# Optimization experiments

Measured on AMD Instinct MI355X. Metric: run time of the kernel, lower is better.

## Reference

```python
import jax, jax.numpy as jnp
import numpy as np

B, S, D, H = 2, 2048, 1024, 16
HD = D // H  # head_dim = 64
ROPE_BASE = 10000.0


def apply_rope(x, positions):
    # x: [B, S, H, HD], positions: [B, S] int. Rotate-half RoPE.
    d = x.shape[-1]
    inv_freq = 1.0 / (ROPE_BASE ** (jnp.arange(0, d, 2, dtype=jnp.float32) / d))  # [d/2]
    ang = positions[..., None].astype(jnp.float32) * inv_freq  # [B, S, d/2]
    cos = jnp.cos(ang)[:, :, None, :]
    sin = jnp.sin(ang)[:, :, None, :]
    x1, x2 = jnp.split(x, 2, axis=-1)
    return jnp.concatenate([x1 * cos - x2 * sin, x2 * cos + x1 * sin], axis=-1).astype(x.dtype)


def setup_inputs() -> dict:
    key = jax.random.key(0)
    k1, k2, k3 = jax.random.split(key, 3)
    inputs = jax.random.normal(k1, (B, S, D), dtype=jnp.float32)
    # nn.Linear weights [out_features, in_features]
    W_in = jax.random.normal(k2, (3 * D, D), dtype=jnp.float32) * (1.0 / np.sqrt(D))
    W_out = jax.random.normal(k3, (D, D), dtype=jnp.float32) * (1.0 / np.sqrt(D))
    positions = jnp.tile(jnp.arange(S, dtype=jnp.int32)[None, :], (B, 1))  # [B, S]
    return {"inputs": inputs, "positions": positions, "W_in": W_in, "W_out": W_out}


def reference(inputs, positions, W_in, W_out):
    # fused QKV projection: [B, S, 3D], head-major layout per rearrange '(heads qkv)'
    qkv = jnp.einsum('bsd,ed->bse', inputs, W_in)
    qkv = qkv.reshape(B, S, H, 3 * HD)
    q, k, v = jnp.split(qkv, 3, axis=-1)  # each [B, S, H, HD]
    q = apply_rope(q, positions)
    k = apply_rope(k, positions)
    # einsum_attention (inference path): scale query, full masked softmax
    q = q / jnp.sqrt(jnp.asarray(HD, dtype=q.dtype))
    scores = jnp.einsum('bqhd,bkhd->bhqk', q, k)  # [B, H, S, S]
    mask = (jnp.arange(S)[None, None, :] <= positions[:, :, None])[:, None, :, :]  # [B,1,S,S]
    big_neg = jnp.finfo(scores.dtype).min
    scores = jnp.where(mask, scores, big_neg)
    attn = jax.nn.softmax(scores, axis=-1)
    x = jnp.einsum('bhqk,bkhd->bqhd', attn, v).reshape(B, S, D)
    return jnp.einsum('bsd,ed->bse', x, W_out)
```

## Files before the change

kernel.cpp:

```cpp
#include <hip/hip_runtime.h>
#include <stdint.h>
#include <math.h>

#define B_ 2
#define S_ 2048
#define D_ 1024
#define H_ 16
#define HD_ 64
#define KVBLK 64

typedef __bf16 bf16_t;
typedef __bf16 bf16x4 __attribute__((ext_vector_type(4)));
typedef __bf16 bf16x8 __attribute__((ext_vector_type(8)));
typedef float f32x4 __attribute__((ext_vector_type(4)));
typedef float f32x16 __attribute__((ext_vector_type(16)));
typedef float float4v __attribute__((ext_vector_type(4)));

#define L2E 1.4426950408889634f
#define NINF (-__builtin_inff())

__device__ __forceinline__ void gload_lds16(const bf16_t* g, bf16_t* l) {
  __builtin_amdgcn_global_load_lds((const __attribute__((address_space(1))) void*)g,
                                   (__attribute__((address_space(3))) void*)l, 16, 0, 0);
}

__device__ __forceinline__ uint32_t packbf(float a, float b) {
  union { __bf16 h[2]; uint32_t u; } cvt;
  cvt.h[0] = (__bf16)a; cvt.h[1] = (__bf16)b;
  return cvt.u;
}

__global__ void cast_bf16_kernel(const float* __restrict__ src, bf16_t* __restrict__ dst, int n4) {
  int i = blockIdx.x * blockDim.x + threadIdx.x;
  int stride = gridDim.x * blockDim.x;
  for (; i < n4; i += stride) {
    float4v f = *(const float4v*)(src + (size_t)i * 4);
    bf16x4 o;
    o[0] = (__bf16)f[0]; o[1] = (__bf16)f[1]; o[2] = (__bf16)f[2]; o[3] = (__bf16)f[3];
    *(bf16x4*)(dst + (size_t)i * 4) = o;
  }
}

template <typename OutT>
__global__ __launch_bounds__(256) void gemm_bt(const bf16_t* __restrict__ A,
                                               const bf16_t* __restrict__ Bm,
                                               OutT* __restrict__ C,
                                               int M, int N, int K) {
  __shared__ bf16_t As[128 * 32];
  __shared__ bf16_t Bs[128 * 32];
  const int t = threadIdx.x;
  const int lane = t & 63, wave = t >> 6;
  const int wr = wave >> 1, wc = wave & 1;
  const int qr = lane & 15, g = lane >> 4;
  const int bm = blockIdx.x, bn = blockIdx.y;

  f32x4 acc[4][4];
#pragma unroll
  for (int m = 0; m < 4; m++)
#pragma unroll
    for (int n = 0; n < 4; n++) acc[m][n] = (f32x4){0.f, 0.f, 0.f, 0.f};

  const bf16_t* Abase = A + (size_t)(bm * 128) * K;
  const bf16_t* Bbase = Bm + (size_t)(bn * 128) * K;
  const int srow = t >> 2;
  const int scol = (t & 3) * 8;

  for (int kk = 0; kk < K; kk += 32) {
    gload_lds16(Abase + (size_t)srow * K + kk + scol,        As + t * 8);
    gload_lds16(Abase + (size_t)(srow + 64) * K + kk + scol, As + 2048 + t * 8);
    gload_lds16(Bbase + (size_t)srow * K + kk + scol,        Bs + t * 8);
    gload_lds16(Bbase + (size_t)(srow + 64) * K + kk + scol, Bs + 2048 + t * 8);
    __syncthreads();
    bf16x8 a[4], b[4];
#pragma unroll
    for (int m = 0; m < 4; m++)
      a[m] = *(const bf16x8*)(As + (wr * 64 + m * 16 + qr) * 32 + g * 8);
#pragma unroll
    for (int n = 0; n < 4; n++)
      b[n] = *(const bf16x8*)(Bs + (wc * 64 + n * 16 + qr) * 32 + g * 8);
#pragma unroll
    for (int m = 0; m < 4; m++)
#pragma unroll
      for (int n = 0; n < 4; n++)
        acc[m][n] = __builtin_amdgcn_mfma_f32_16x16x32_bf16(a[m], b[n], acc[m][n], 0, 0, 0);
    __syncthreads();
  }

#pragma unroll
  for (int m = 0; m < 4; m++) {
    int row0 = bm * 128 + wr * 64 + m * 16 + g * 4;
#pragma unroll
    for (int n = 0; n < 4; n++) {
      int col = bn * 128 + wc * 64 + n * 16 + qr;
#pragma unroll
      for (int r = 0; r < 4; r++)
        C[(size_t)(row0 + r) * N + col] = (OutT)acc[m][n][r];
    }
  }
}

template <typename OutT>
__global__ __launch_bounds__(512, 2) void gemm256(const bf16_t* __restrict__ A,
                                                  const bf16_t* __restrict__ Bm,
                                                  OutT* __restrict__ C,
                                                  int M, int N, int K) {
  __shared__ bf16_t As[2][256 * 64];
  __shared__ bf16_t Bs[2][256 * 64];
  const int t = threadIdx.x;
  const int lane = t & 63, wid = t >> 6;
  const int qr = lane & 15, g = lane >> 4;
  const int wm = wid >> 2, wn = wid & 3;
  const int bm = blockIdx.x, bn = blockIdx.y;
  const int NT = K >> 6;

  const bf16_t* Ab = A + (size_t)(bm * 256) * K;
  const bf16_t* Bb = Bm + (size_t)(bn * 256) * K;

  const bf16_t* srcA[4];
  const bf16_t* srcB[4];
  int ldsOff[4];
#pragma unroll
  for (int i = 0; i < 4; i++) {
    int e = t + 512 * i;
    int row = e >> 3, cs = e & 7;
    int gcol = (cs ^ (row & 7)) * 8;
    srcA[i] = Ab + (size_t)row * K + gcol;
    srcB[i] = Bb + (size_t)row * K + gcol;
    ldsOff[i] = e * 8;
  }

  f32x4 acc[8][4];
#pragma unroll
  for (int m = 0; m < 8; m++)
#pragma unroll
    for (int n = 0; n < 4; n++) acc[m][n] = (f32x4){0.f, 0.f, 0.f, 0.f};

#define RD(buf_, r_, k_) (*(const bf16x8*)((buf_) + (r_) * 64 + ((((k_) * 4 + g) ^ ((r_) & 7)) * 8)))

#pragma unroll
  for (int i = 0; i < 4; i++) gload_lds16(srcA[i], As[0] + ldsOff[i]);
#pragma unroll
  for (int i = 0; i < 4; i++) gload_lds16(srcB[i], Bs[0] + ldsOff[i]);
#pragma unroll
  for (int i = 0; i < 4; i++) gload_lds16(srcA[i] + 64, As[1] + ldsOff[i]);
#pragma unroll
  for (int i = 0; i < 4; i++) gload_lds16(srcB[i] + 64, Bs[1] + ldsOff[i]);

  for (int T = 0; T < NT; ++T) {
    bf16_t* A_c = As[T & 1];
    bf16_t* B_c = Bs[T & 1];
    if (T + 1 < NT) asm volatile("s_waitcnt vmcnt(8)" ::: "memory");
    else            asm volatile("s_waitcnt vmcnt(0)" ::: "memory");
    __builtin_amdgcn_sched_barrier(0);
    __builtin_amdgcn_s_barrier();

    const bool st = (T + 2 < NT);
    const int kt2 = (T + 2) * 64;

    bf16x8 alo[4][2], ahi[4][2], bfr[4][2];

#pragma unroll
    for (int m = 0; m < 4; m++) {
      int r = wm * 128 + m * 16 + qr;
      alo[m][0] = RD(A_c, r, 0); alo[m][1] = RD(A_c, r, 1);
    }
#pragma unroll
    for (int n = 0; n < 2; n++) {
      int r = wn * 64 + n * 16 + qr;
      bfr[n][0] = RD(B_c, r, 0); bfr[n][1] = RD(B_c, r, 1);
    }
    __builtin_amdgcn_s_barrier();
    __builtin_amdgcn_s_setprio(1);
#pragma unroll
    for (int m = 0; m < 4; m++)
#pragma unroll
      for (int n = 0; n < 2; n++)
#pragma unroll
        for (int k = 0; k < 2; k++)
          acc[m][n] = __builtin_amdgcn_mfma_f32_16x16x32_bf16(alo[m][k], bfr[n][k], acc[m][n], 0, 0, 0);
    __builtin_amdgcn_s_setprio(0);
    __builtin_amdgcn_s_barrier();

#pragma unroll
    for (int n = 2; n < 4; n++) {
      int r = wn * 64 + n * 16 + qr;
      bfr[n][0] = RD(B_c, r, 0); bfr[n][1] = RD(B_c, r, 1);
    }
    if (st) {
      gload_lds16(srcA[0] + kt2, A_c + ldsOff[0]);
      gload_lds16(srcA[2] + kt2, A_c + ldsOff[2]);
    }
    __builtin_amdgcn_s_barrier();
    __builtin_amdgcn_s_setprio(1);
#pragma unroll
    for (int m = 0; m < 4; m++)
#pragma unroll
      for (int n = 2; n < 4; n++)
#pragma unroll
        for (int k = 0; k < 2; k++)
          acc[m][n] = __builtin_amdgcn_mfma_f32_16x16x32_bf16(alo[m][k], bfr[n][k], acc[m][n], 0, 0, 0);
    __builtin_amdgcn_s_setprio(0);
    __builtin_amdgcn_s_barrier();

#pragma unroll
    for (int m = 0; m < 4; m++) {
      int r = wm * 128 + (m + 4) * 16 + qr;
      ahi[m][0] = RD(A_c, r, 0); ahi[m][1] = RD(A_c, r, 1);
    }
    if (st) {
      gload_lds16(srcB[0] + kt2, B_c + ldsOff[0]);
      gload_lds16(srcB[1] + kt2, B_c + ldsOff[1]);
      gload_lds16(srcB[2] + kt2, B_c + ldsOff[2]);
      gload_lds16(srcB[3] + kt2, B_c + ldsOff[3]);
    }
    __builtin_amdgcn_s_barrier();
    __builtin_amdgcn_s_setprio(1);
#pragma unroll
    for (int m = 0; m < 4; m++)
#pragma unroll
      for (int n = 0; n < 2; n++)
#pragma unroll
        for (int k = 0; k < 2; k++)
          acc[m + 4][n] = __builtin_amdgcn_mfma_f32_16x16x32_bf16(ahi[m][k], bfr[n][k], acc[m + 4][n], 0, 0, 0);
    __builtin_amdgcn_s_setprio(0);
    __builtin_amdgcn_s_barrier();

    if (st) {
      gload_lds16(srcA[1] + kt2, A_c + ldsOff[1]);
      gload_lds16(srcA[3] + kt2, A_c + ldsOff[3]);
    }
    __builtin_amdgcn_s_barrier();
    __builtin_amdgcn_s_setprio(1);
#pragma unroll
    for (int m = 0; m < 4; m++)
#pragma unroll
      for (int n = 2; n < 4; n++)
#pragma unroll
        for (int k = 0; k < 2; k++)
          acc[m + 4][n] = __builtin_amdgcn_mfma_f32_16x16x32_bf16(ahi[m][k], bfr[n][k], acc[m + 4][n], 0, 0, 0);
    __builtin_amdgcn_s_setprio(0);
    __builtin_amdgcn_s_barrier();
  }
#undef RD

#pragma unroll
  for (int m = 0; m < 8; m++) {
    int row0 = bm * 256 + wm * 128 + m * 16 + g * 4;
#pragma unroll
    for (int n = 0; n < 4; n++) {
      int col = bn * 256 + wn * 64 + n * 16 + qr;
#pragma unroll
      for (int r = 0; r < 4; r++)
        C[(size_t)(row0 + r) * N + col] = (OutT)acc[m][n][r];
    }
  }
}

__global__ void rope_qk_kernel(const bf16_t* __restrict__ qkv, const int* __restrict__ pos,
                               bf16_t* __restrict__ Q, bf16_t* __restrict__ Ko) {
  int idx = blockIdx.x * blockDim.x + threadIdx.x;
  if (idx >= B_ * S_ * H_ * 32) return;
  int i = idx & 31;
  int h = (idx >> 5) & (H_ - 1);
  int bs = idx >> 9;
  const bf16_t* row = qkv + (size_t)bs * (3 * D_) + h * 192;
  float q1 = (float)row[i], q2 = (float)row[i + 32];
  float k1 = (float)row[64 + i], k2 = (float)row[96 + i];
  int p = pos[bs];
  float inv = exp2f(-(float)i * (13.287712379549449f / 32.0f));
  float ang = (float)p * inv;
  float sn, cs;
  sincosf(ang, &sn, &cs);
  float qo1 = (q1 * cs - q2 * sn) * 0.125f;
  float qo2 = (q2 * cs + q1 * sn) * 0.125f;
  float ko1 = k1 * cs - k2 * sn;
  float ko2 = k2 * cs + k1 * sn;
  int b = bs >> 11, s = bs & (S_ - 1);
  size_t o = ((size_t)(b * H_ + h) * S_ + s) * HD_ + i;
  Q[o] = (__bf16)qo1;  Q[o + 32] = (__bf16)qo2;
  Ko[o] = (__bf16)ko1; Ko[o + 32] = (__bf16)ko2;
}

__global__ __launch_bounds__(256) void v_transpose_kernel(const bf16_t* __restrict__ qkv,
                                                          bf16_t* __restrict__ Vt) {
  __shared__ bf16_t tile[64][72];
  int t = threadIdx.x;
  int s0 = blockIdx.x * 64;
  int h = blockIdx.y, b = blockIdx.z;
  int sl = t >> 4;
  int cb = (t & 15) * 4;
#pragma unroll
  for (int it = 0; it < 4; it++) {
    int s = sl + it * 16;
    const bf16_t* src = qkv + (size_t)(b * S_ + s0 + s) * (3 * D_) + h * 192 + 128 + cb;
    bf16x4 v = *(const bf16x4*)src;
    tile[cb + 0][s] = v[0]; tile[cb + 1][s] = v[1];
    tile[cb + 2][s] = v[2]; tile[cb + 3][s] = v[3];
  }
  __syncthreads();
#pragma unroll
  for (int it = 0; it < 4; it++) {
    int d = sl + it * 16;
    bf16x4 v;
    v[0] = tile[d][cb]; v[1] = tile[d][cb + 1]; v[2] = tile[d][cb + 2]; v[3] = tile[d][cb + 3];
    *(bf16x4*)(Vt + ((size_t)((b * H_ + h) * HD_ + d)) * S_ + s0 + cb) = v;
  }
}

__global__ __launch_bounds__(256) void attn_kernel(const bf16_t* __restrict__ Q,
                                                   const bf16_t* __restrict__ K,
                                                   const bf16_t* __restrict__ Vt,
                                                   const int* __restrict__ pos,
                                                   bf16_t* __restrict__ O) {
  __shared__ bf16_t Ks[2][64 * 64];
  __shared__ bf16_t Vs[2][64 * 64];

  const int t = threadIdx.x;
  const int lane = t & 63, wv = t >> 6;
  const int l31 = lane & 31, hi = lane >> 5;

  const int bid = blockIdx.x;
  const int bh = (bid & 7) * 4 + ((bid >> 3) & 3);
  const int qblk = 15 - (bid >> 5);
  const int b = bh >> 4, h = bh & 15;
  const int q0 = qblk * 128;

  const bf16_t* Qb = Q + (size_t)bh * (S_ * HD_);
  const bf16_t* Kb = K + (size_t)bh * (S_ * HD_);
  const bf16_t* Vb = Vt + (size_t)bh * (HD_ * S_);

  const int qrow = q0 + wv * 32 + l31;
  bf16x8 qf[4];
#pragma unroll
  for (int c = 0; c < 4; c++)
    qf[c] = *(const bf16x8*)(Qb + (size_t)qrow * HD_ + c * 16 + hi * 8);

  const int prow = pos[b * S_ + qrow];
  int wmin = prow;
#pragma unroll
  for (int off = 1; off < 32; off <<= 1) wmin = min(wmin, __shfl_xor(wmin, off));

  int mp = max(pos[b * S_ + q0 + lane], pos[b * S_ + q0 + 64 + lane]);
#pragma unroll
  for (int off = 1; off < 64; off <<= 1) mp = max(mp, __shfl_xor(mp, off));
  const int ntiles = min(S_ / KVBLK, (mp >> 6) + 1);

  const int r0 = t >> 3, c0 = t & 7;
  const int r1 = (t + 256) >> 3, c1 = t & 7;
  const bf16_t* KgA = Kb + (size_t)r0 * HD_ + ((c0 ^ (r0 & 7)) * 8);
  const bf16_t* KgB = Kb + (size_t)r1 * HD_ + ((c1 ^ (r1 & 7)) * 8);
  const bf16_t* VgA = Vb + (size_t)r0 * S_ + ((c0 ^ (r0 & 7)) * 8);
  const bf16_t* VgB = Vb + (size_t)r1 * S_ + ((c1 ^ (r1 & 7)) * 8);
  const int ldsA = t * 8, ldsB = (t + 256) * 8;

  f32x16 oT[2];
#pragma unroll
  for (int dt = 0; dt < 2; dt++)
#pragma unroll
    for (int r = 0; r < 16; r++) oT[dt][r] = 0.f;
  float m_run = NINF, l_run = 0.f;

  gload_lds16(KgA, Ks[0] + ldsA);
  gload_lds16(KgB, Ks[0] + ldsB);
  gload_lds16(VgA, Vs[0] + ldsA);
  gload_lds16(VgB, Vs[0] + ldsB);
  __syncthreads();

  for (int kt = 0; kt < ntiles; ++kt) {
    const int k0 = kt * KVBLK;
    const int cur = kt & 1;
    if (kt + 1 < ntiles) {
      const int kn = (kt + 1) * KVBLK;
      gload_lds16(KgA + (size_t)kn * HD_, Ks[cur ^ 1] + ldsA);
      gload_lds16(KgB + (size_t)kn * HD_, Ks[cur ^ 1] + ldsB);
      gload_lds16(VgA + kn, Vs[cur ^ 1] + ldsA);
      gload_lds16(VgB + kn, Vs[cur ^ 1] + ldsB);
    }
    const bf16_t* Kc = Ks[cur];
    const bf16_t* Vc = Vs[cur];

    f32x16 s0, s1;
#pragma unroll
    for (int r = 0; r < 16; r++) { s0[r] = 0.f; s1[r] = 0.f; }
    __builtin_amdgcn_s_setprio(1);
#pragma unroll
    for (int c = 0; c < 4; c++) {
      const int c2 = c * 2 + hi;
      const int kr0 = l31;
      const int kr1 = 32 + l31;
      bf16x8 kf0 = *(const bf16x8*)(Kc + kr0 * 64 + ((c2 ^ (kr0 & 7)) * 8));
      bf16x8 kf1 = *(const bf16x8*)(Kc + kr1 * 64 + ((c2 ^ (kr1 & 7)) * 8));
      s0 = __builtin_amdgcn_mfma_f32_32x32x16_bf16(kf0, qf[c], s0, 0, 0, 0);
      s1 = __builtin_amdgcn_mfma_f32_32x32x16_bf16(kf1, qf[c], s1, 0, 0, 0);
    }
    __builtin_amdgcn_s_setprio(0);

    float p0[16], p1[16];
    if (k0 + 63 > wmin) {
#pragma unroll
      for (int r = 0; r < 16; r++) {
        int koff = (r & 3) + 8 * (r >> 2) + 4 * hi;
        p0[r] = (k0 + koff <= prow) ? s0[r] : NINF;
        p1[r] = (k0 + 32 + koff <= prow) ? s1[r] : NINF;
      }
    } else {
#pragma unroll
      for (int r = 0; r < 16; r++) { p0[r] = s0[r]; p1[r] = s1[r]; }
    }

    float tm = NINF;
#pragma unroll
    for (int r = 0; r < 16; r++) tm = fmaxf(tm, fmaxf(p0[r], p1[r]));
    tm = fmaxf(tm, __shfl_xor(tm, 32));
    if (__any(tm > m_run + 8.0f)) {
      float mn = fmaxf(fmaxf(m_run, tm), -1e30f);
      float scale = exp2f((m_run - mn) * L2E);
      l_run *= scale;
#pragma unroll
      for (int dt = 0; dt < 2; dt++)
#pragma unroll
        for (int r = 0; r < 16; r++) oT[dt][r] *= scale;
      m_run = mn;
    }
    const float mnl = m_run * L2E;
    float rs = 0.f;
#pragma unroll
    for (int r = 0; r < 16; r++) {
      p0[r] = exp2f(p0[r] * L2E - mnl);
      p1[r] = exp2f(p1[r] * L2E - mnl);
      rs += p0[r] + p1[r];
    }
    rs += __shfl_xor(rs, 32);
    l_run += rs;

#pragma unroll
    for (int kc = 0; kc < 4; kc++) {
      const float* P = (kc < 2) ? p0 : p1;
      const int rb = (kc & 1) * 8;
      uint32_t xa0 = packbf(P[rb + 0], P[rb + 1]);
      uint32_t xa1 = packbf(P[rb + 2], P[rb + 3]);
      uint32_t xb0 = packbf(P[rb + 4], P[rb + 5]);
      uint32_t xb1 = packbf(P[rb + 6], P[rb + 7]);
      uint32_t sa0 = (uint32_t)__shfl_xor((int)xa0, 32);
      uint32_t sa1 = (uint32_t)__shfl_xor((int)xa1, 32);
      uint32_t sb0 = (uint32_t)__shfl_xor((int)xb0, 32);
      uint32_t sb1 = (uint32_t)__shfl_xor((int)xb1, 32);
      union { uint32_t u[4]; bf16x8 v; } pf;
      pf.u[0] = hi ? sb0 : xa0;
      pf.u[1] = hi ? sb1 : xa1;
      pf.u[2] = hi ? xb0 : sa0;
      pf.u[3] = hi ? xb1 : sa1;
      __builtin_amdgcn_s_setprio(1);
#pragma unroll
      for (int dt = 0; dt < 2; dt++) {
        const int vr = dt * 32 + l31;
        const int c2 = kc * 2 + hi;
        bf16x8 vf = *(const bf16x8*)(Vc + vr * 64 + ((c2 ^ (vr & 7)) * 8));
        oT[dt] = __builtin_amdgcn_mfma_f32_32x32x16_bf16(vf, pf.v, oT[dt], 0, 0, 0);
      }
      __builtin_amdgcn_s_setprio(0);
    }

    __syncthreads();
  }

  const float rl = (l_run > 0.f) ? 1.0f / l_run : 0.f;
  bf16_t* Ot = (bf16_t*)Ks + wv * 2048;
#pragma unroll
  for (int dt = 0; dt < 2; dt++)
#pragma unroll
    for (int r = 0; r < 16; r++) {
      int chunk = dt * 4 + (r >> 2);
      int el = (r & 3) + 4 * hi;
      Ot[l31 * 64 + ((chunk ^ (l31 & 7)) * 8) + el] = (__bf16)(oT[dt][r] * rl);
    }
  __syncthreads();
#pragma unroll
  for (int it = 0; it < 4; it++) {
    int qr2 = (lane >> 3) + it * 8;
    int cc = lane & 7;
    bf16x8 v = *(const bf16x8*)(Ot + qr2 * 64 + ((cc ^ (qr2 & 7)) * 8));
    *(bf16x8*)(&O[(size_t)(b * S_ + q0 + wv * 32 + qr2) * D_ + h * 64 + cc * 8]) = v;
  }
}

extern "C" void kernel_launch(void* const* d_in, const int* in_sizes, int n_in,
                              void* d_out, int out_size, void* d_ws, size_t ws_size,
                              hipStream_t stream) {
  const float* inputs = (const float*)d_in[0];
  const int* positions = (const int*)d_in[1];
  const float* W_in = (const float*)d_in[2];
  const float* W_out = (const float*)d_in[3];
  float* out = (float*)d_out;

  bf16_t* X_bf = (bf16_t*)d_ws;
  bf16_t* Win_bf = X_bf + (size_t)4096 * 1024;
  bf16_t* Wout_bf = Win_bf + (size_t)3072 * 1024;
  bf16_t* qkv_bf = Wout_bf + (size_t)1024 * 1024;
  bf16_t* Qb = qkv_bf + (size_t)4096 * 3072;
  bf16_t* Kb = Qb + (size_t)B_ * H_ * S_ * HD_;
  bf16_t* Vtb = Kb + (size_t)B_ * H_ * S_ * HD_;
  bf16_t* Ob = Vtb + (size_t)B_ * H_ * S_ * HD_;

  cast_bf16_kernel<<<dim3(2048), dim3(256), 0, stream>>>(inputs, X_bf, (4096 * 1024) / 4);
  cast_bf16_kernel<<<dim3(2048), dim3(256), 0, stream>>>(W_in, Win_bf, (3072 * 1024) / 4);
  cast_bf16_kernel<<<dim3(1024), dim3(256), 0, stream>>>(W_out, Wout_bf, (1024 * 1024) / 4);

  gemm256<bf16_t><<<dim3(16, 12), dim3(512), 0, stream>>>(X_bf, Win_bf, qkv_bf, 4096, 3072, 1024);

  rope_qk_kernel<<<dim3((B_ * S_ * H_ * 32) / 256), dim3(256), 0, stream>>>(qkv_bf, positions, Qb, Kb);
  v_transpose_kernel<<<dim3(S_ / 64, H_, B_), dim3(256), 0, stream>>>(qkv_bf, Vtb);

  attn_kernel<<<dim3(512), dim3(256), 0, stream>>>(Qb, Kb, Vtb, positions, Ob);

  gemm_bt<float><<<dim3(32, 8), dim3(256), 0, stream>>>(Ob, Wout_bf, out, 4096, 1024, 1024);
}
```

Before: 160.1 us.

## Split attention KV range across two blocks with merge kernel; fuse casts

Attention query blocks whose causal range spans more than 16 KV tiles are now split into two halves run by separate blocks. Each half writes unnormalized partial outputs plus running max and sum, and a new merge kernel combines the two halves. This doubles the grid to balance the causal workload and fill more compute units, at the cost of an extra kernel launch, partial-output traffic and bf16 rounding of the partials. The three fp32-to-bf16 cast launches are also fused into one kernel.

```diff
diff --git a/kernel.cpp b/kernel.cpp
--- a/kernel.cpp
+++ b/kernel.cpp
@@ -30,14 +30,21 @@
   return cvt.u;
 }
 
-__global__ void cast_bf16_kernel(const float* __restrict__ src, bf16_t* __restrict__ dst, int n4) {
+__global__ void cast3_bf16_kernel(const float* __restrict__ s0, bf16_t* __restrict__ d0, int n0,
+                                  const float* __restrict__ s1, bf16_t* __restrict__ d1, int n1,
+                                  const float* __restrict__ s2, bf16_t* __restrict__ d2, int n2) {
   int i = blockIdx.x * blockDim.x + threadIdx.x;
   int stride = gridDim.x * blockDim.x;
-  for (; i < n4; i += stride) {
-    float4v f = *(const float4v*)(src + (size_t)i * 4);
+  int tot = n0 + n1 + n2;
+  for (; i < tot; i += stride) {
+    const float* s; bf16_t* d; int j = i;
+    if (j < n0) { s = s0; d = d0; }
+    else if ((j -= n0) < n1) { s = s1; d = d1; }
+    else { j -= n1; s = s2; d = d2; }
+    float4v f = *(const float4v*)(s + (size_t)j * 4);
     bf16x4 o;
     o[0] = (__bf16)f[0]; o[1] = (__bf16)f[1]; o[2] = (__bf16)f[2]; o[3] = (__bf16)f[3];
-    *(bf16x4*)(dst + (size_t)i * 4) = o;
+    *(bf16x4*)(d + (size_t)j * 4) = o;
   }
 }
 
@@ -311,7 +318,10 @@
                                                    const bf16_t* __restrict__ K,
                                                    const bf16_t* __restrict__ Vt,
                                                    const int* __restrict__ pos,
-                                                   bf16_t* __restrict__ O) {
+                                                   bf16_t* __restrict__ O,
+                                                   bf16_t* __restrict__ Opart,
+                                                   float* __restrict__ Mst,
+                                                   float* __restrict__ Lst) {
   __shared__ bf16_t Ks[2][64 * 64];
   __shared__ bf16_t Vs[2][64 * 64];
 
@@ -321,7 +331,9 @@
 
   const int bid = blockIdx.x;
   const int bh = (bid & 7) * 4 + ((bid >> 3) & 3);
-  const int qblk = 15 - (bid >> 5);
+  const int v5 = bid >> 5;
+  const int qblk = 15 - (v5 >> 1);
+  const int half = v5 & 1;
   const int b = bh >> 4, h = bh & 15;
   const int q0 = qblk * 128;
 
@@ -330,20 +342,26 @@
   const bf16_t* Vb = Vt + (size_t)bh * (HD_ * S_);
 
   const int qrow = q0 + wv * 32 + l31;
+
+  const int prow = pos[b * S_ + qrow];
+  int wmin = prow;
+#pragma unroll
+  for (int off = 1; off < 32; off <<= 1) wmin = min(wmin, __shfl_xor(wmin, off));
+
+  int mp = max(pos[b * S_ + q0 + lane], pos[b * S_ + q0 + 64 + lane]);
+#pragma unroll
+  for (int off = 1; off < 64; off <<= 1) mp = max(mp, __shfl_xor(mp, off));
+  const int nt = min(S_ / KVBLK, (mp >> 6) + 1);
+
+  const int t0 = half * 16;
+  const int t1 = min(nt, t0 + 16);
+  if (t0 >= t1) return;
+  const bool needs_merge = (nt > 16);
+
   bf16x8 qf[4];
 #pragma unroll
   for (int c = 0; c < 4; c++)
     qf[c] = *(const bf16x8*)(Qb + (size_t)qrow * HD_ + c * 16 + hi * 8);
-
-  const int prow = pos[b * S_ + qrow];
-  int wmin = prow;
-#pragma unroll
-  for (int off = 1; off < 32; off <<= 1) wmin = min(wmin, __shfl_xor(wmin, off));
-
-  int mp = max(pos[b * S_ + q0 + lane], pos[b * S_ + q0 + 64 + lane]);
-#pragma unroll
-  for (int off = 1; off < 64; off <<= 1) mp = max(mp, __shfl_xor(mp, off));
-  const int ntiles = min(S_ / KVBLK, (mp >> 6) + 1);
 
   const int r0 = t >> 3, c0 = t & 7;
   const int r1 = (t + 256) >> 3, c1 = t & 7;
@@ -360,16 +378,19 @@
     for (int r = 0; r < 16; r++) oT[dt][r] = 0.f;
   float m_run = NINF, l_run = 0.f;
 
-  gload_lds16(KgA, Ks[0] + ldsA);
-  gload_lds16(KgB, Ks[0] + ldsB);
-  gload_lds16(VgA, Vs[0] + ldsA);
-  gload_lds16(VgB, Vs[0] + ldsB);
+  {
+    const int kn = t0 * KVBLK;
+    gload_lds16(KgA + (size_t)kn * HD_, Ks[0] + ldsA);
+    gload_lds16(KgB + (size_t)kn * HD_, Ks[0] + ldsB);
+    gload_lds16(VgA + kn, Vs[0] + ldsA);
+    gload_lds16(VgB + kn, Vs[0] + ldsB);
+  }
   __syncthreads();
 
-  for (int kt = 0; kt < ntiles; ++kt) {
+  for (int kt = t0; kt < t1; ++kt) {
     const int k0 = kt * KVBLK;
     const int cur = kt & 1;
-    if (kt + 1 < ntiles) {
+    if (kt + 1 < t1) {
       const int kn = (kt + 1) * KVBLK;
       gload_lds16(KgA + (size_t)kn * HD_, Ks[cur ^ 1] + ldsA);
       gload_lds16(KgB + (size_t)kn * HD_, Ks[cur ^ 1] + ldsB);
@@ -422,7 +443,7 @@
         for (int r = 0; r < 16; r++) oT[dt][r] *= scale;
       m_run = mn;
     }
-    const float mnl = m_run * L2E;
+    const float mnl = (m_run == NINF) ? 3.0e38f : m_run * L2E;
     float rs = 0.f;
 #pragma unroll
     for (int r = 0; r < 16; r++) {
@@ -464,7 +485,7 @@
     __syncthreads();
   }
 
-  const float rl = (l_run > 0.f) ? 1.0f / l_run : 0.f;
+  const float rl = needs_merge ? 1.0f : ((l_run > 0.f) ? 1.0f / l_run : 0.f);
   bf16_t* Ot = (bf16_t*)Ks + wv * 2048;
 #pragma unroll
   for (int dt = 0; dt < 2; dt++)
@@ -475,12 +496,75 @@
       Ot[l31 * 64 + ((chunk ^ (l31 & 7)) * 8) + el] = (__bf16)(oT[dt][r] * rl);
     }
   __syncthreads();
-#pragma unroll
-  for (int it = 0; it < 4; it++) {
-    int qr2 = (lane >> 3) + it * 8;
-    int cc = lane & 7;
-    bf16x8 v = *(const bf16x8*)(Ot + qr2 * 64 + ((cc ^ (qr2 & 7)) * 8));
-    *(bf16x8*)(&O[(size_t)(b * S_ + q0 + wv * 32 + qr2) * D_ + h * 64 + cc * 8]) = v;
+  if (needs_merge) {
+    bf16_t* dst = Opart + (((size_t)(half * 32 + bh) * 16 + qblk) * 128) * 64;
+#pragma unroll
+    for (int it = 0; it < 4; it++) {
+      int qr2 = (lane >> 3) + it * 8;
+      int cc = lane & 7;
+      bf16x8 vv = *(const bf16x8*)(Ot + qr2 * 64 + ((cc ^ (qr2 & 7)) * 8));
+      *(bf16x8*)(&dst[(size_t)(wv * 32 + qr2) * 64 + cc * 8]) = vv;
+    }
+    if (hi == 0) {
+      size_t sidx = ((size_t)(half * 32 + bh) * 16 + qblk) * 128 + wv * 32 + l31;
+      Mst[sidx] = m_run;
+      Lst[sidx] = l_run;
+    }
+  } else {
+#pragma unroll
+    for (int it = 0; it < 4; it++) {
+      int qr2 = (lane >> 3) + it * 8;
+      int cc = lane & 7;
+      bf16x8 vv = *(const bf16x8*)(Ot + qr2 * 64 + ((cc ^ (qr2 & 7)) * 8));
+      *(bf16x8*)(&O[(size_t)(b * S_ + q0 + wv * 32 + qr2) * D_ + h * 64 + cc * 8]) = vv;
+    }
+  }
+}
+
+__global__ __launch_bounds__(256) void attn_merge_kernel(const bf16_t* __restrict__ Opart,
+                                                         const float* __restrict__ Mst,
+                                                         const float* __restrict__ Lst,
+                                                         const int* __restrict__ pos,
+                                                         bf16_t* __restrict__ O) {
+  __shared__ int wmax_s[4];
+  const int t = threadIdx.x;
+  const int bid = blockIdx.x;
+  const int bh = (bid & 7) * 4 + ((bid >> 3) & 3);
+  const int qblk = 15 - (bid >> 5);
+  const int b = bh >> 4, h = bh & 15;
+  const int q0 = qblk * 128;
+
+  int p = pos[b * S_ + q0 + (t & 127)];
+#pragma unroll
+  for (int off = 1; off < 64; off <<= 1) p = max(p, __shfl_xor(p, off));
+  if ((t & 63) == 0) wmax_s[t >> 6] = p;
+  __syncthreads();
+  int mp = max(max(wmax_s[0], wmax_s[1]), max(wmax_s[2], wmax_s[3]));
+  if ((mp >> 6) + 1 <= 16) return;
+
+  const int r = t >> 1, dh = (t & 1) * 32;
+  const size_t s0i = ((size_t)(0 * 32 + bh) * 16 + qblk) * 128 + r;
+  const size_t s1i = ((size_t)(1 * 32 + bh) * 16 + qblk) * 128 + r;
+  float m0 = Mst[s0i], l0 = Lst[s0i];
+  float m1 = Mst[s1i], l1 = Lst[s1i];
+  float m = fmaxf(fmaxf(m0, m1), -1e30f);
+  float w0 = exp2f((m0 - m) * L2E);
+  float w1 = exp2f((m1 - m) * L2E);
+  float lt = l0 * w0 + l1 * w1;
+  float rl = (lt > 0.f) ? 1.0f / lt : 0.f;
+  w0 *= rl; w1 *= rl;
+  const bf16_t* pa = Opart + s0i * 64 + dh;
+  const bf16_t* pb = Opart + s1i * 64 + dh;
+  bf16_t* dst = O + (size_t)(b * S_ + q0 + r) * D_ + h * 64 + dh;
+#pragma unroll
+  for (int c = 0; c < 4; c++) {
+    bf16x8 a = *(const bf16x8*)(pa + c * 8);
+    bf16x8 bb = *(const bf16x8*)(pb + c * 8);
+    bf16x8 o;
+#pragma unroll
+    for (int j = 0; j < 8; j++)
+      o[j] = (__bf16)((float)a[j] * w0 + (float)bb[j] * w1);
+    *(bf16x8*)(dst + c * 8) = o;
   }
 }
 
@@ -502,16 +586,22 @@
   bf16_t* Vtb = Kb + (size_t)B_ * H_ * S_ * HD_;
   bf16_t* Ob = Vtb + (size_t)B_ * H_ * S_ * HD_;
 
-  cast_bf16_kernel<<<dim3(2048), dim3(256), 0, stream>>>(inputs, X_bf, (4096 * 1024) / 4);
-  cast_bf16_kernel<<<dim3(2048), dim3(256), 0, stream>>>(W_in, Win_bf, (3072 * 1024) / 4);
-  cast_bf16_kernel<<<dim3(1024), dim3(256), 0, stream>>>(W_out, Wout_bf, (1024 * 1024) / 4);
+  bf16_t* Opart = qkv_bf;
+  float* Mst = (float*)(qkv_bf + (size_t)2 * 32 * 16 * 128 * 64);
+  float* Lst = Mst + (size_t)2 * 32 * 16 * 128;
+
+  cast3_bf16_kernel<<<dim3(2048), dim3(256), 0, stream>>>(
+      inputs, X_bf, (4096 * 1024) / 4,
+      W_in, Win_bf, (3072 * 1024) / 4,
+      W_out, Wout_bf, (1024 * 1024) / 4);
 
   gemm256<bf16_t><<<dim3(16, 12), dim3(512), 0, stream>>>(X_bf, Win_bf, qkv_bf, 4096, 3072, 1024);
 
   rope_qk_kernel<<<dim3((B_ * S_ * H_ * 32) / 256), dim3(256), 0, stream>>>(qkv_bf, positions, Qb, Kb);
   v_transpose_kernel<<<dim3(S_ / 64, H_, B_), dim3(256), 0, stream>>>(qkv_bf, Vtb);
 
-  attn_kernel<<<dim3(512), dim3(256), 0, stream>>>(Qb, Kb, Vtb, positions, Ob);
+  attn_kernel<<<dim3(1024), dim3(256), 0, stream>>>(Qb, Kb, Vtb, positions, Ob, Opart, Mst, Lst);
+  attn_merge_kernel<<<dim3(512), dim3(256), 0, stream>>>(Opart, Mst, Lst, positions, Ob);
 
   gemm_bt<float><<<dim3(32, 8), dim3(256), 0, stream>>>(Ob, Wout_bf, out, 4096, 1024, 1024);
 }
```

Measured after the change: 152.9 us. 4.5% less time.
